# Performance work log

Hardware: AMD Instinct MI355X
Metric: run time of the kernel (lower is better)

## Reference

```python
import jax, jax.numpy as jnp
import numpy as np

B, T, D = 2, 2048, 1024
E, H, K = 8, 2048, 2  # n_experts, expert_dim, n_active_experts


def setup_inputs() -> dict:
    key = jax.random.key(0)
    ks = jax.random.split(key, 5)
    s = 0.02
    return {
        "x": jax.random.normal(ks[0], (B, T, D), dtype=jnp.float32),
        "gate_w": jax.random.normal(ks[1], (E, D), dtype=jnp.float32) * s,
        "w1": jax.random.normal(ks[2], (E, H, D), dtype=jnp.float32) * s,
        "w2": jax.random.normal(ks[3], (E, D, H), dtype=jnp.float32) * s,
        "w3": jax.random.normal(ks[4], (E, H, D), dtype=jnp.float32) * s,
    }


def reference(x, gate_w, w1, w2, w3):
    Bb, Tt, Dd = x.shape
    xf = x.reshape(-1, Dd)                       # [N, D]
    logits = xf @ gate_w.T                       # [N, E]
    probs = jax.nn.softmax(logits, axis=-1)
    vals, idx = jax.lax.top_k(probs, K)          # [N, K]
    w = vals / (vals.sum(-1, keepdims=True) + 1e-8)
    onehot = jax.nn.one_hot(idx, E, dtype=xf.dtype)  # [N, K, E]
    comb = jnp.einsum('nk,nke->ne', w, onehot)   # per-token per-expert combine weight
    # Dense expert eval (same math as masked loop): SwiGLU per expert
    h = jnp.einsum('nd,ehd->neh', xf, w1)        # [N, E, H]
    g = jnp.einsum('nd,ehd->neh', xf, w3)
    eo = jnp.einsum('neh,edh->ned', jax.nn.silu(h) * g, w2)  # [N, E, D]
    out = jnp.einsum('ned,ne->nd', eo, comb)
    return out.reshape(Bb, Tt, Dd)
```

## Files before the change

### kernel.cpp

```cpp
#include <hip/hip_runtime.h>
#include <stdint.h>

#define N_TOK 4096
#define DIM   1024
#define NEXP  8
#define HDIM  2048
#define NSLOT 8192

typedef __attribute__((ext_vector_type(8))) short  short8;
typedef __attribute__((ext_vector_type(4))) float  f32x4;

__device__ inline unsigned short f2bf(float f) {
  union { float f; uint32_t u; } v; v.f = f;
  uint32_t u = v.u;
  u += 0x7fffu + ((u >> 16) & 1u);
  return (unsigned short)(u >> 16);
}

__device__ inline void gload_lds16(const void* g, void* l) {
  __builtin_amdgcn_global_load_lds(
      (const __attribute__((address_space(1))) uint32_t*)g,
      (__attribute__((address_space(3))) uint32_t*)l, 16, 0, 0);
}

__global__ __launch_bounds__(256) void cvt_all_kernel(const float* __restrict__ x,
                                                      const float* __restrict__ w1,
                                                      const float* __restrict__ w2,
                                                      const float* __restrict__ w3,
                                                      unsigned short* __restrict__ xb,
                                                      unsigned short* __restrict__ w1b,
                                                      unsigned short* __restrict__ w2b,
                                                      unsigned short* __restrict__ w3b) {
  const int NX = N_TOK * DIM / 4;
  const int NW = NEXP * HDIM * DIM / 4;
  int i = blockIdx.x * blockDim.x + threadIdx.x;
  int stride = gridDim.x * blockDim.x;
  int total = NX + 3 * NW;
  for (; i < total; i += stride) {
    const float* s; unsigned short* d; int j;
    if (i < NX)               { s = x;  d = xb;  j = i; }
    else if (i < NX + NW)     { s = w1; d = w1b; j = i - NX; }
    else if (i < NX + 2 * NW) { s = w2; d = w2b; j = i - NX - NW; }
    else                      { s = w3; d = w3b; j = i - NX - 2 * NW; }
    float4 f = reinterpret_cast<const float4*>(s)[j];
    ushort4 o;
    o.x = f2bf(f.x); o.y = f2bf(f.y); o.z = f2bf(f.z); o.w = f2bf(f.w);
    reinterpret_cast<ushort4*>(d)[j] = o;
  }
}

__global__ __launch_bounds__(256) void gate_kernel(const float* __restrict__ x,
                                                   const float* __restrict__ gw,
                                                   int* __restrict__ tok_e,
                                                   float* __restrict__ tok_w) {
  __shared__ float gws[NEXP * DIM];
  int tid = threadIdx.x;
  for (int i = tid; i < NEXP * DIM; i += 256) gws[i] = gw[i];
  __syncthreads();
  int lane = tid & 63;
  int token = blockIdx.x * 4 + (tid >> 6);
  const float* xr = x + (size_t)token * DIM;
  float acc[NEXP];
#pragma unroll
  for (int e = 0; e < NEXP; ++e) acc[e] = 0.f;
  for (int i = 0; i < DIM / 64; ++i) {
    float xv = xr[i * 64 + lane];
#pragma unroll
    for (int e = 0; e < NEXP; ++e) acc[e] += xv * gws[e * DIM + i * 64 + lane];
  }
#pragma unroll
  for (int off = 32; off > 0; off >>= 1) {
#pragma unroll
    for (int e = 0; e < NEXP; ++e) acc[e] += __shfl_xor(acc[e], off);
  }
  if (lane == 0) {
    float m = acc[0];
#pragma unroll
    for (int e = 1; e < NEXP; ++e) m = fmaxf(m, acc[e]);
    float ex[NEXP], Z = 0.f;
#pragma unroll
    for (int e = 0; e < NEXP; ++e) { ex[e] = expf(acc[e] - m); Z += ex[e]; }
    int b0 = 0; float v0 = ex[0];
#pragma unroll
    for (int e = 1; e < NEXP; ++e) if (ex[e] > v0) { v0 = ex[e]; b0 = e; }
    int b1 = -1; float v1 = -1.f;
#pragma unroll
    for (int e = 0; e < NEXP; ++e) if (e != b0 && ex[e] > v1) { v1 = ex[e]; b1 = e; }
    float p0 = v0 / Z, p1 = v1 / Z;
    float s = p0 + p1 + 1e-8f;
    tok_e[token * 2 + 0] = b0; tok_e[token * 2 + 1] = b1;
    tok_w[token * 2 + 0] = p0 / s; tok_w[token * 2 + 1] = p1 / s;
  }
}

__global__ __launch_bounds__(1024) void route_kernel(const int* __restrict__ tok_e,
                                                     const float* __restrict__ tok_w,
                                                     int* __restrict__ slot_tok,
                                                     float* __restrict__ slot_w,
                                                     int* __restrict__ cnt_g,
                                                     int* __restrict__ offs_g) {
  __shared__ int cnt[NEXP], offs[NEXP], cur[NEXP];
  int tid = threadIdx.x;
  if (tid < NEXP) cnt[tid] = 0;
  __syncthreads();
  for (int n = tid; n < N_TOK; n += 1024) {
    atomicAdd(&cnt[tok_e[2 * n]], 1);
    atomicAdd(&cnt[tok_e[2 * n + 1]], 1);
  }
  __syncthreads();
  if (tid == 0) {
    int o = 0;
    for (int e = 0; e < NEXP; ++e) { offs[e] = o; cur[e] = o; o += cnt[e]; }
    for (int e = 0; e < NEXP; ++e) { cnt_g[e] = cnt[e]; offs_g[e] = offs[e]; }
  }
  __syncthreads();
  for (int n = tid; n < N_TOK; n += 1024) {
#pragma unroll
    for (int k = 0; k < 2; ++k) {
      int e = tok_e[2 * n + k];
      int p = atomicAdd(&cur[e], 1);
      slot_tok[p] = n;
      slot_w[p] = tok_w[2 * n + k];
    }
  }
}

__global__ __launch_bounds__(512, 2) void gemm1_kernel(const unsigned short* __restrict__ xb,
                                                       const unsigned short* __restrict__ w1b,
                                                       const unsigned short* __restrict__ w3b,
                                                       const int* __restrict__ slot_tok,
                                                       const int* __restrict__ cnt_g,
                                                       const int* __restrict__ offs_g,
                                                       unsigned short* __restrict__ hidden) {
  const int ROWT = 16;
  const int COLT = HDIM / 128;
  int bid = blockIdx.x;
  int e  = bid / (ROWT * COLT);
  int rt = (bid / COLT) % ROWT;
  int ct = bid % COLT;
  int cnt = cnt_g[e];
  if (rt * 256 >= cnt) return;
  int rowBase = offs_g[e] + rt * 256;

  __shared__ alignas(16) unsigned short As[2][256 * 64];
  __shared__ alignas(16) unsigned short B1s[2][128 * 64];
  __shared__ alignas(16) unsigned short B3s[2][128 * 64];
  __shared__ int toks[256];

  int tid = threadIdx.x;
  if (tid < 256) {
    int slot = rowBase + tid; if (slot > NSLOT - 1) slot = NSLOT - 1;
    toks[tid] = slot_tok[slot];
  }
  __syncthreads();

  int wave = tid >> 6, lane = tid & 63;
  int wr = (wave >> 1) * 64;
  int wc = (wave & 1) * 64;
  int sub = lane >> 3;
  int swcol = (((lane & 7) ^ sub) << 3);

  const size_t wbase = (size_t)e * HDIM * DIM;
  const unsigned short* aptr[4];
  const unsigned short* b1ptr[2];
  const unsigned short* b3ptr[2];
#pragma unroll
  for (int i = 0; i < 4; ++i) {
    int r = (wave + i * 8) * 8 + sub;
    aptr[i] = xb + (size_t)toks[r] * DIM + swcol;
  }
#pragma unroll
  for (int i = 0; i < 2; ++i) {
    int r = (wave + i * 8) * 8 + sub;
    b1ptr[i] = w1b + wbase + (size_t)(ct * 128 + r) * DIM + swcol;
    b3ptr[i] = w3b + wbase + (size_t)(ct * 128 + r) * DIM + swcol;
  }

  f32x4 hacc[4][4], gacc[4][4];
#pragma unroll
  for (int m = 0; m < 4; ++m)
#pragma unroll
    for (int n = 0; n < 4; ++n) {
      hacc[m][n] = (f32x4){0.f, 0.f, 0.f, 0.f};
      gacc[m][n] = (f32x4){0.f, 0.f, 0.f, 0.f};
    }

  gload_lds16(aptr[0], &As[0][(wave + 0) * 512]);
  gload_lds16(aptr[1], &As[0][(wave + 8) * 512]);
  gload_lds16(aptr[2], &As[0][(wave + 16) * 512]);
  gload_lds16(aptr[3], &As[0][(wave + 24) * 512]);
  gload_lds16(b1ptr[0], &B1s[0][wave * 512]);
  gload_lds16(b1ptr[1], &B1s[0][(wave + 8) * 512]);
  gload_lds16(b3ptr[0], &B3s[0][wave * 512]);
  gload_lds16(b3ptr[1], &B3s[0][(wave + 8) * 512]);

  const int NKT = DIM / 64;
  int key = (lane & 7) << 3;
  int l15 = lane & 15;
  int pc0 = ((lane >> 4) * 8) ^ key;
  int pc1 = (32 + (lane >> 4) * 8) ^ key;

  for (int kt = 0; kt < NKT; ++kt) {
    int c = kt & 1;
    int nk = (kt + 1) * 64;
    bool pre = (kt + 1 < NKT);

    __builtin_amdgcn_sched_barrier(0);
    __builtin_amdgcn_s_barrier();
    __builtin_amdgcn_sched_barrier(0);
    if (pre) {
      gload_lds16(aptr[0] + nk, &As[c ^ 1][(wave + 0) * 512]);
      gload_lds16(aptr[1] + nk, &As[c ^ 1][(wave + 8) * 512]);
      asm volatile("s_waitcnt vmcnt(4)" ::: "memory");
    } else {
      asm volatile("s_waitcnt vmcnt(2)" ::: "memory");
    }
    __builtin_amdgcn_sched_barrier(0);
    __builtin_amdgcn_s_barrier();
    __builtin_amdgcn_sched_barrier(0);

    short8 a0[4], a1[4], bv[4];
#pragma unroll
    for (int m = 0; m < 4; ++m)
      a0[m] = *(const short8*)&As[c][(wr + m * 16 + l15) * 64 + pc0];
#pragma unroll
    for (int n = 0; n < 4; ++n)
      bv[n] = *(const short8*)&B1s[c][(wc + n * 16 + l15) * 64 + pc0];
    if (pre) {
      gload_lds16(aptr[2] + nk, &As[c ^ 1][(wave + 16) * 512]);
      gload_lds16(aptr[3] + nk, &As[c ^ 1][(wave + 24) * 512]);
    }
    __builtin_amdgcn_s_setprio(1);
#pragma unroll
    for (int m = 0; m < 4; ++m)
#pragma unroll
      for (int n = 0; n < 4; ++n)
        hacc[m][n] = __builtin_amdgcn_mfma_f32_16x16x32_bf16(a0[m], bv[n], hacc[m][n], 0, 0, 0);
    __builtin_amdgcn_s_setprio(0);

#pragma unroll
    for (int m = 0; m < 4; ++m)
      a1[m] = *(const short8*)&As[c][(wr + m * 16 + l15) * 64 + pc1];
#pragma unroll
    for (int n = 0; n < 4; ++n)
      bv[n] = *(const short8*)&B1s[c][(wc + n * 16 + l15) * 64 + pc1];
    if (pre) {
      gload_lds16(b1ptr[0] + nk, &B1s[c ^ 1][wave * 512]);
      gload_lds16(b1ptr[1] + nk, &B1s[c ^ 1][(wave + 8) * 512]);
    }
    __builtin_amdgcn_s_setprio(1);
#pragma unroll
    for (int m = 0; m < 4; ++m)
#pragma unroll
      for (int n = 0; n < 4; ++n)
        hacc[m][n] = __builtin_amdgcn_mfma_f32_16x16x32_bf16(a1[m], bv[n], hacc[m][n], 0, 0, 0);
    __builtin_amdgcn_s_setprio(0);

    if (pre) asm volatile("s_waitcnt vmcnt(6)" ::: "memory");
    else     asm volatile("s_waitcnt vmcnt(0)" ::: "memory");
    __builtin_amdgcn_sched_barrier(0);
    __builtin_amdgcn_s_barrier();
    __builtin_amdgcn_sched_barrier(0);

#pragma unroll
    for (int n = 0; n < 4; ++n)
      bv[n] = *(const short8*)&B3s[c][(wc + n * 16 + l15) * 64 + pc0];
    if (pre) {
      gload_lds16(b3ptr[0] + nk, &B3s[c ^ 1][wave * 512]);
      gload_lds16(b3ptr[1] + nk, &B3s[c ^ 1][(wave + 8) * 512]);
    }
    __builtin_amdgcn_s_setprio(1);
#pragma unroll
    for (int m = 0; m < 4; ++m)
#pragma unroll
      for (int n = 0; n < 4; ++n)
        gacc[m][n] = __builtin_amdgcn_mfma_f32_16x16x32_bf16(a0[m], bv[n], gacc[m][n], 0, 0, 0);
    __builtin_amdgcn_s_setprio(0);

#pragma unroll
    for (int n = 0; n < 4; ++n)
      bv[n] = *(const short8*)&B3s[c][(wc + n * 16 + l15) * 64 + pc1];
    __builtin_amdgcn_s_setprio(1);
#pragma unroll
    for (int m = 0; m < 4; ++m)
#pragma unroll
      for (int n = 0; n < 4; ++n)
        gacc[m][n] = __builtin_amdgcn_mfma_f32_16x16x32_bf16(a1[m], bv[n], gacc[m][n], 0, 0, 0);
    __builtin_amdgcn_s_setprio(0);
  }

  int cbase = ct * 128 + wc;
#pragma unroll
  for (int m = 0; m < 4; ++m) {
#pragma unroll
    for (int q = 0; q < 4; ++q) {
      int r = wr + m * 16 + ((lane >> 4) * 4 + q);
      if (rt * 256 + r < cnt) {
        size_t rowoff = (size_t)(rowBase + r) * HDIM + cbase;
#pragma unroll
        for (int n = 0; n < 4; ++n) {
          float h = hacc[m][n][q], g = gacc[m][n][q];
          float val = (h / (1.f + expf(-h))) * g;
          hidden[rowoff + n * 16 + (lane & 15)] = f2bf(val);
        }
      }
    }
  }
}

__global__ __launch_bounds__(256, 2) void gemm2_kernel(const unsigned short* __restrict__ hidden,
                                                       const unsigned short* __restrict__ w2b,
                                                       const int* __restrict__ slot_tok,
                                                       const float* __restrict__ slot_w,
                                                       const int* __restrict__ cnt_g,
                                                       const int* __restrict__ offs_g,
                                                       float* __restrict__ out) {
  const int ROWT = 32;
  const int COLT = DIM / 128;
  int bid = blockIdx.x;
  int e  = bid / (ROWT * COLT);
  int rt = (bid / COLT) % ROWT;
  int ct = bid % COLT;
  int cnt = cnt_g[e];
  if (rt * 128 >= cnt) return;
  int rowBase = offs_g[e] + rt * 128;

  __shared__ alignas(16) unsigned short As[2][128 * 64];
  __shared__ alignas(16) unsigned short Bs[2][128 * 64];
  __shared__ int   toks[128];
  __shared__ float wgt[128];

  int tid = threadIdx.x;
  if (tid < 128) {
    int slot = rowBase + tid; if (slot > NSLOT - 1) slot = NSLOT - 1;
    toks[tid] = slot_tok[slot];
    wgt[tid]  = slot_w[slot];
  }
  __syncthreads();

  int wave = tid >> 6, lane = tid & 63;
  int wr = (wave >> 1) * 64, wc = (wave & 1) * 64;
  int sub = lane >> 3;
  int swcol = (((lane & 7) ^ sub) << 3);

  const size_t w2base = (size_t)e * DIM * HDIM;
  const unsigned short* aptr[4];
  const unsigned short* bptr[4];
#pragma unroll
  for (int i = 0; i < 4; ++i) {
    int r = (wave + i * 4) * 8 + sub;
    int rg = rowBase + r; if (rg > NSLOT - 1) rg = NSLOT - 1;
    aptr[i] = hidden + (size_t)rg * HDIM + swcol;
    bptr[i] = w2b + w2base + (size_t)(ct * 128 + r) * HDIM + swcol;
  }

  f32x4 acc[4][4];
#pragma unroll
  for (int m = 0; m < 4; ++m)
#pragma unroll
    for (int n = 0; n < 4; ++n) acc[m][n] = (f32x4){0.f, 0.f, 0.f, 0.f};

#pragma unroll
  for (int i = 0; i < 4; ++i)
    gload_lds16(aptr[i], &As[0][(wave + i * 4) * 512]);
#pragma unroll
  for (int i = 0; i < 4; ++i)
    gload_lds16(bptr[i], &Bs[0][(wave + i * 4) * 512]);

  const int NKT = HDIM / 64;
  int key = (lane & 7) << 3;
  int l15 = lane & 15;
  int pc0 = ((lane >> 4) * 8) ^ key;
  int pc1 = (32 + (lane >> 4) * 8) ^ key;

  for (int kt = 0; kt < NKT; ++kt) {
    int c = kt & 1;
    int nk = (kt + 1) * 64;
    bool pre = (kt + 1 < NKT);

    __builtin_amdgcn_sched_barrier(0);
    __builtin_amdgcn_s_barrier();
    __builtin_amdgcn_sched_barrier(0);
    if (pre) {
#pragma unroll
      for (int i = 0; i < 4; ++i)
        gload_lds16(aptr[i] + nk, &As[c ^ 1][(wave + i * 4) * 512]);
      asm volatile("s_waitcnt vmcnt(4)" ::: "memory");
    } else {
      asm volatile("s_waitcnt vmcnt(0)" ::: "memory");
    }
    __builtin_amdgcn_sched_barrier(0);
    __builtin_amdgcn_s_barrier();
    __builtin_amdgcn_sched_barrier(0);

    short8 a[4], b[4];
#pragma unroll
    for (int m = 0; m < 4; ++m)
      a[m] = *(const short8*)&As[c][(wr + m * 16 + l15) * 64 + pc0];
#pragma unroll
    for (int n = 0; n < 4; ++n)
      b[n] = *(const short8*)&Bs[c][(wc + n * 16 + l15) * 64 + pc0];
    if (pre) {
#pragma unroll
      for (int i = 0; i < 4; ++i)
        gload_lds16(bptr[i] + nk, &Bs[c ^ 1][(wave + i * 4) * 512]);
    }
    __builtin_amdgcn_s_setprio(1);
#pragma unroll
    for (int m = 0; m < 4; ++m)
#pragma unroll
      for (int n = 0; n < 4; ++n)
        acc[m][n] = __builtin_amdgcn_mfma_f32_16x16x32_bf16(a[m], b[n], acc[m][n], 0, 0, 0);
    __builtin_amdgcn_s_setprio(0);

#pragma unroll
    for (int m = 0; m < 4; ++m)
      a[m] = *(const short8*)&As[c][(wr + m * 16 + l15) * 64 + pc1];
#pragma unroll
    for (int n = 0; n < 4; ++n)
      b[n] = *(const short8*)&Bs[c][(wc + n * 16 + l15) * 64 + pc1];
    __builtin_amdgcn_s_setprio(1);
#pragma unroll
    for (int m = 0; m < 4; ++m)
#pragma unroll
      for (int n = 0; n < 4; ++n)
        acc[m][n] = __builtin_amdgcn_mfma_f32_16x16x32_bf16(a[m], b[n], acc[m][n], 0, 0, 0);
    __builtin_amdgcn_s_setprio(0);
  }

  int cbase = ct * 128 + wc;
#pragma unroll
  for (int m = 0; m < 4; ++m) {
#pragma unroll
    for (int q = 0; q < 4; ++q) {
      int r = wr + m * 16 + ((lane >> 4) * 4 + q);
      if (rt * 128 + r < cnt) {
        float w = wgt[r];
        float* orow = out + (size_t)toks[r] * DIM + cbase;
#pragma unroll
        for (int n = 0; n < 4; ++n)
          unsafeAtomicAdd(&orow[n * 16 + (lane & 15)], acc[m][n][q] * w);
      }
    }
  }
}

extern "C" void kernel_launch(void* const* d_in, const int* in_sizes, int n_in,
                              void* d_out, int out_size, void* d_ws, size_t ws_size,
                              hipStream_t stream) {
  const float* x  = (const float*)d_in[0];
  const float* gw = (const float*)d_in[1];
  const float* w1 = (const float*)d_in[2];
  const float* w2 = (const float*)d_in[3];
  const float* w3 = (const float*)d_in[4];
  float* out = (float*)d_out;

  uint8_t* ws = (uint8_t*)d_ws;
  size_t off = 0;
  auto alloc = [&](size_t bytes) -> void* {
    void* p = ws + off; off += (bytes + 255) & ~255ull; return p;
  };
  unsigned short* xb     = (unsigned short*)alloc((size_t)N_TOK * DIM * 2);
  unsigned short* w1b    = (unsigned short*)alloc((size_t)NEXP * HDIM * DIM * 2);
  unsigned short* w3b    = (unsigned short*)alloc((size_t)NEXP * HDIM * DIM * 2);
  unsigned short* w2b    = (unsigned short*)alloc((size_t)NEXP * DIM * HDIM * 2);
  unsigned short* hidden = (unsigned short*)alloc((size_t)NSLOT * HDIM * 2);
  int*   tok_e    = (int*)alloc(N_TOK * 2 * 4);
  float* tok_w    = (float*)alloc(N_TOK * 2 * 4);
  int*   slot_tok = (int*)alloc(NSLOT * 4);
  float* slot_w   = (float*)alloc(NSLOT * 4);
  int*   cnt_g    = (int*)alloc(NEXP * 4);
  int*   offs_g   = (int*)alloc(NEXP * 4);

  hipMemsetAsync(d_out, 0, (size_t)out_size * sizeof(float), stream);

  cvt_all_kernel<<<2048, 256, 0, stream>>>(x, w1, w2, w3, xb, w1b, w2b, w3b);

  gate_kernel<<<N_TOK / 4, 256, 0, stream>>>(x, gw, tok_e, tok_w);
  route_kernel<<<1, 1024, 0, stream>>>(tok_e, tok_w, slot_tok, slot_w, cnt_g, offs_g);
  gemm1_kernel<<<NEXP * 16 * (HDIM / 128), 512, 0, stream>>>(
      xb, w1b, w3b, slot_tok, cnt_g, offs_g, hidden);
  gemm2_kernel<<<NEXP * 32 * (DIM / 128), 256, 0, stream>>>(
      hidden, w2b, slot_tok, slot_w, cnt_g, offs_g, out);
}
```

Baseline: 460.5 us.

## Pad expert segments to tile multiples and launch compact tile lists for GEMMs

The route kernel now pads each expert's slot range to a multiple of 256 and emits explicit tile lists (expert, row base) for both GEMMs. The GEMMs launch grids sized to the maximum tile count instead of every expert×row-tile combination, so far fewer blocks exit early. Per-row bounds checks in the epilogues are dropped. Padded slots point at token 0 with zero weight, which costs some wasted MMA work and zero-valued atomics on token 0's output row.

Result: slower. 520.5 us (+13.0%).

```diff
diff --git a/kernel.cpp b/kernel.cpp
--- a/kernel.cpp
+++ b/kernel.cpp
@@ -6,6 +6,9 @@
 #define NEXP  8
 #define HDIM  2048
 #define NSLOT 8192
+#define PADSLOT 10240
+#define MAXT1 40
+#define MAXT2 80
 
 typedef __attribute__((ext_vector_type(8))) short  short8;
 typedef __attribute__((ext_vector_type(4))) float  f32x4;
@@ -97,9 +100,13 @@
                                                      const float* __restrict__ tok_w,
                                                      int* __restrict__ slot_tok,
                                                      float* __restrict__ slot_w,
-                                                     int* __restrict__ cnt_g,
-                                                     int* __restrict__ offs_g) {
-  __shared__ int cnt[NEXP], offs[NEXP], cur[NEXP];
+                                                     int* __restrict__ tile1_e,
+                                                     int* __restrict__ tile1_rb,
+                                                     int* __restrict__ tile2_e,
+                                                     int* __restrict__ tile2_rb,
+                                                     int* __restrict__ ntile_g) {
+  __shared__ int cnt[NEXP], cur[NEXP];
+  __shared__ int total_sh;
   int tid = threadIdx.x;
   if (tid < NEXP) cnt[tid] = 0;
   __syncthreads();
@@ -109,10 +116,20 @@
   }
   __syncthreads();
   if (tid == 0) {
-    int o = 0;
-    for (int e = 0; e < NEXP; ++e) { offs[e] = o; cur[e] = o; o += cnt[e]; }
-    for (int e = 0; e < NEXP; ++e) { cnt_g[e] = cnt[e]; offs_g[e] = offs[e]; }
-  }
+    int o = 0, n1 = 0, n2 = 0;
+    for (int e = 0; e < NEXP; ++e) {
+      cur[e] = o;
+      int padded = (cnt[e] + 255) & ~255;
+      for (int rb = o; rb < o + padded; rb += 256) { tile1_e[n1] = e; tile1_rb[n1] = rb; ++n1; }
+      for (int rb = o; rb < o + padded; rb += 128) { tile2_e[n2] = e; tile2_rb[n2] = rb; ++n2; }
+      o += padded;
+    }
+    ntile_g[0] = n1; ntile_g[1] = n2;
+    total_sh = o;
+  }
+  __syncthreads();
+  int total = total_sh;
+  for (int s = tid; s < total; s += 1024) { slot_tok[s] = 0; slot_w[s] = 0.f; }
   __syncthreads();
   for (int n = tid; n < N_TOK; n += 1024) {
 #pragma unroll
@@ -129,18 +146,15 @@
                                                        const unsigned short* __restrict__ w1b,
                                                        const unsigned short* __restrict__ w3b,
                                                        const int* __restrict__ slot_tok,
-                                                       const int* __restrict__ cnt_g,
-                                                       const int* __restrict__ offs_g,
+                                                       const int* __restrict__ tile1_e,
+                                                       const int* __restrict__ tile1_rb,
+                                                       const int* __restrict__ ntile_g,
                                                        unsigned short* __restrict__ hidden) {
-  const int ROWT = 16;
-  const int COLT = HDIM / 128;
-  int bid = blockIdx.x;
-  int e  = bid / (ROWT * COLT);
-  int rt = (bid / COLT) % ROWT;
-  int ct = bid % COLT;
-  int cnt = cnt_g[e];
-  if (rt * 256 >= cnt) return;
-  int rowBase = offs_g[e] + rt * 256;
+  int tile = blockIdx.x >> 4;
+  int ct   = blockIdx.x & 15;
+  if (tile >= ntile_g[0]) return;
+  int e = tile1_e[tile];
+  int rowBase = tile1_rb[tile];
 
   __shared__ alignas(16) unsigned short As[2][256 * 64];
   __shared__ alignas(16) unsigned short B1s[2][128 * 64];
@@ -148,10 +162,7 @@
   __shared__ int toks[256];
 
   int tid = threadIdx.x;
-  if (tid < 256) {
-    int slot = rowBase + tid; if (slot > NSLOT - 1) slot = NSLOT - 1;
-    toks[tid] = slot_tok[slot];
-  }
+  if (tid < 256) toks[tid] = slot_tok[rowBase + tid];
   __syncthreads();
 
   int wave = tid >> 6, lane = tid & 63;
@@ -295,14 +306,12 @@
 #pragma unroll
     for (int q = 0; q < 4; ++q) {
       int r = wr + m * 16 + ((lane >> 4) * 4 + q);
-      if (rt * 256 + r < cnt) {
-        size_t rowoff = (size_t)(rowBase + r) * HDIM + cbase;
-#pragma unroll
-        for (int n = 0; n < 4; ++n) {
-          float h = hacc[m][n][q], g = gacc[m][n][q];
-          float val = (h / (1.f + expf(-h))) * g;
-          hidden[rowoff + n * 16 + (lane & 15)] = f2bf(val);
-        }
+      size_t rowoff = (size_t)(rowBase + r) * HDIM + cbase;
+#pragma unroll
+      for (int n = 0; n < 4; ++n) {
+        float h = hacc[m][n][q], g = gacc[m][n][q];
+        float val = (h / (1.f + expf(-h))) * g;
+        hidden[rowoff + n * 16 + (lane & 15)] = f2bf(val);
       }
     }
   }
@@ -312,18 +321,15 @@
                                                        const unsigned short* __restrict__ w2b,
                                                        const int* __restrict__ slot_tok,
                                                        const float* __restrict__ slot_w,
-                                                       const int* __restrict__ cnt_g,
-                                                       const int* __restrict__ offs_g,
+                                                       const int* __restrict__ tile2_e,
+                                                       const int* __restrict__ tile2_rb,
+                                                       const int* __restrict__ ntile_g,
                                                        float* __restrict__ out) {
-  const int ROWT = 32;
-  const int COLT = DIM / 128;
-  int bid = blockIdx.x;
-  int e  = bid / (ROWT * COLT);
-  int rt = (bid / COLT) % ROWT;
-  int ct = bid % COLT;
-  int cnt = cnt_g[e];
-  if (rt * 128 >= cnt) return;
-  int rowBase = offs_g[e] + rt * 128;
+  int tile = blockIdx.x >> 3;
+  int ct   = blockIdx.x & 7;
+  if (tile >= ntile_g[1]) return;
+  int e = tile2_e[tile];
+  int rowBase = tile2_rb[tile];
 
   __shared__ alignas(16) unsigned short As[2][128 * 64];
   __shared__ alignas(16) unsigned short Bs[2][128 * 64];
@@ -332,9 +338,8 @@
 
   int tid = threadIdx.x;
   if (tid < 128) {
-    int slot = rowBase + tid; if (slot > NSLOT - 1) slot = NSLOT - 1;
-    toks[tid] = slot_tok[slot];
-    wgt[tid]  = slot_w[slot];
+    toks[tid] = slot_tok[rowBase + tid];
+    wgt[tid]  = slot_w[rowBase + tid];
   }
   __syncthreads();
 
@@ -349,8 +354,7 @@
 #pragma unroll
   for (int i = 0; i < 4; ++i) {
     int r = (wave + i * 4) * 8 + sub;
-    int rg = rowBase + r; if (rg > NSLOT - 1) rg = NSLOT - 1;
-    aptr[i] = hidden + (size_t)rg * HDIM + swcol;
+    aptr[i] = hidden + (size_t)(rowBase + r) * HDIM + swcol;
     bptr[i] = w2b + w2base + (size_t)(ct * 128 + r) * HDIM + swcol;
   }
 
@@ -434,13 +438,11 @@
 #pragma unroll
     for (int q = 0; q < 4; ++q) {
       int r = wr + m * 16 + ((lane >> 4) * 4 + q);
-      if (rt * 128 + r < cnt) {
-        float w = wgt[r];
-        float* orow = out + (size_t)toks[r] * DIM + cbase;
-#pragma unroll
-        for (int n = 0; n < 4; ++n)
-          unsafeAtomicAdd(&orow[n * 16 + (lane & 15)], acc[m][n][q] * w);
-      }
+      float w = wgt[r];
+      float* orow = out + (size_t)toks[r] * DIM + cbase;
+#pragma unroll
+      for (int n = 0; n < 4; ++n)
+        unsafeAtomicAdd(&orow[n * 16 + (lane & 15)], acc[m][n][q] * w);
     }
   }
 }
@@ -464,22 +466,26 @@
   unsigned short* w1b    = (unsigned short*)alloc((size_t)NEXP * HDIM * DIM * 2);
   unsigned short* w3b    = (unsigned short*)alloc((size_t)NEXP * HDIM * DIM * 2);
   unsigned short* w2b    = (unsigned short*)alloc((size_t)NEXP * DIM * HDIM * 2);
-  unsigned short* hidden = (unsigned short*)alloc((size_t)NSLOT * HDIM * 2);
+  unsigned short* hidden = (unsigned short*)alloc((size_t)PADSLOT * HDIM * 2);
   int*   tok_e    = (int*)alloc(N_TOK * 2 * 4);
   float* tok_w    = (float*)alloc(N_TOK * 2 * 4);
-  int*   slot_tok = (int*)alloc(NSLOT * 4);
-  float* slot_w   = (float*)alloc(NSLOT * 4);
-  int*   cnt_g    = (int*)alloc(NEXP * 4);
-  int*   offs_g   = (int*)alloc(NEXP * 4);
+  int*   slot_tok = (int*)alloc(PADSLOT * 4);
+  float* slot_w   = (float*)alloc(PADSLOT * 4);
+  int*   tile1_e  = (int*)alloc(MAXT1 * 4);
+  int*   tile1_rb = (int*)alloc(MAXT1 * 4);
+  int*   tile2_e  = (int*)alloc(MAXT2 * 4);
+  int*   tile2_rb = (int*)alloc(MAXT2 * 4);
+  int*   ntile_g  = (int*)alloc(2 * 4);
 
   hipMemsetAsync(d_out, 0, (size_t)out_size * sizeof(float), stream);
 
   cvt_all_kernel<<<2048, 256, 0, stream>>>(x, w1, w2, w3, xb, w1b, w2b, w3b);
 
   gate_kernel<<<N_TOK / 4, 256, 0, stream>>>(x, gw, tok_e, tok_w);
-  route_kernel<<<1, 1024, 0, stream>>>(tok_e, tok_w, slot_tok, slot_w, cnt_g, offs_g);
-  gemm1_kernel<<<NEXP * 16 * (HDIM / 128), 512, 0, stream>>>(
-      xb, w1b, w3b, slot_tok, cnt_g, offs_g, hidden);
-  gemm2_kernel<<<NEXP * 32 * (DIM / 128), 256, 0, stream>>>(
-      hidden, w2b, slot_tok, slot_w, cnt_g, offs_g, out);
-}
+  route_kernel<<<1, 1024, 0, stream>>>(tok_e, tok_w, slot_tok, slot_w,
+                                       tile1_e, tile1_rb, tile2_e, tile2_rb, ntile_g);
+  gemm1_kernel<<<MAXT1 * 16, 512, 0, stream>>>(
+      xb, w1b, w3b, slot_tok, tile1_e, tile1_rb, ntile_g, hidden);
+  gemm2_kernel<<<MAXT2 * 8, 256, 0, stream>>>(
+      hidden, w2b, slot_tok, slot_w, tile2_e, tile2_rb, ntile_g, out);
+}
```
